# Kernel tuning notes

Hardware: AMD Instinct MI355X
Metric: run time of the kernel (lower is better)

The kernel has to match this reference:

```python
import jax, jax.numpy as jnp
import numpy as np

B, T, C = 4, 2048, 2048
H, KV, HD = 16, 4, 128  # n_head, n_kv_head, head_dim
G = H // KV             # query heads per kv head


def _rope(t, cos, sin):
    # t: [B, T, h, HD]; cos/sin: [T, HD//2] -> broadcast as [1, T, 1, HD//2]
    tr = t.reshape(t.shape[:-1] + (HD // 2, 2))
    t_r, t_i = tr[..., 0], tr[..., 1]
    c = cos[None, :, None, :]
    s = sin[None, :, None, :]
    o_r = t_r * c - t_i * s
    o_i = t_r * s + t_i * c
    return jnp.stack((o_r, o_i), axis=-1).reshape(t.shape)


def setup_inputs() -> dict:
    key = jax.random.key(0)
    ks = jax.random.split(key, 7)
    sc = 0.02
    return {
        "x": jax.random.normal(ks[0], (B, T, C), jnp.float32),
        "cos_freqs": jnp.cos(jnp.outer(jnp.arange(T, dtype=jnp.float32),
                                       1.0 / (10000.0 ** (jnp.arange(HD // 2, dtype=jnp.float32) * 2 / HD)))),
        "sin_freqs": jnp.sin(jnp.outer(jnp.arange(T, dtype=jnp.float32),
                                       1.0 / (10000.0 ** (jnp.arange(HD // 2, dtype=jnp.float32) * 2 / HD)))),
        "wq": jax.random.normal(ks[1], (H * HD, C), jnp.float32) * sc,
        "wk": jax.random.normal(ks[2], (KV * HD, C), jnp.float32) * sc,
        "wv": jax.random.normal(ks[3], (KV * HD, C), jnp.float32) * sc,
        "wo": jax.random.normal(ks[4], (C, H * HD), jnp.float32) * sc,
    }


def reference(x, cos_freqs, sin_freqs, wq, wk, wv, wo):
    # projections (Linear with bias=False: y = x @ W.T)
    q = (x @ wq.T).reshape(B, T, H, HD)
    k = (x @ wk.T).reshape(B, T, KV, HD)
    v = (x @ wv.T).reshape(B, T, KV, HD)
    q, k = _rope(q, cos_freqs, sin_freqs), _rope(k, cos_freqs, sin_freqs)
    # GQA attention without materializing repeated K/V: group q heads per kv head
    qg = q.reshape(B, T, KV, G, HD).transpose(0, 2, 3, 1, 4)  # [B,KV,G,T,HD]
    kh = k.transpose(0, 2, 1, 3)                              # [B,KV,T,HD]
    vh = v.transpose(0, 2, 1, 3)                              # [B,KV,T,HD]
    scale = 1.0 / jnp.sqrt(jnp.float32(HD))
    scores = jnp.einsum('bkgtd,bksd->bkgts', qg, kh) * scale  # [B,KV,G,T,T]
    mask = jnp.tril(jnp.ones((T, T), dtype=bool))
    scores = jnp.where(mask, scores, jnp.float32(-jnp.inf))
    attn = jax.nn.softmax(scores, axis=-1)
    out = jnp.einsum('bkgts,bksd->bkgtd', attn, vh)           # [B,KV,G,T,HD]
    out = out.transpose(0, 3, 1, 2, 4).reshape(B, T, H * HD)
    return out @ wo.T
```

## Files before the change

kernel.cpp:

```cpp
#include <hip/hip_runtime.h>
#include <hip/hip_bf16.h>
#include <math.h>

typedef __attribute__((ext_vector_type(8))) short short8;
typedef __attribute__((ext_vector_type(4))) float floatx4;

__device__ __forceinline__ float bf2f(unsigned short u) {
  union { unsigned int i; float f; } x; x.i = ((unsigned int)u) << 16; return x.f;
}
__device__ __forceinline__ unsigned short f2bf(float f) {
  union { float f; unsigned int i; } x; x.f = f;
  unsigned int r = x.i + 0x7FFFu + ((x.i >> 16) & 1u);
  return (unsigned short)(r >> 16);
}
__device__ __forceinline__ unsigned int pack2bf(float a, float b) {
  return (unsigned int)f2bf(a) | ((unsigned int)f2bf(b) << 16);
}
__device__ __forceinline__ void gl16(const void* g, void* l) {
  __builtin_amdgcn_global_load_lds(
      (const __attribute__((address_space(1))) unsigned int*)g,
      (__attribute__((address_space(3))) unsigned int*)l, 16, 0, 0);
}

__global__ void cvt_f32_bf16(const float* __restrict__ in, unsigned short* __restrict__ out, int n4) {
  int i = blockIdx.x * blockDim.x + threadIdx.x;
  if (i >= n4) return;
  float4 v = ((const float4*)in)[i];
  ushort4 o;
  o.x = f2bf(v.x); o.y = f2bf(v.y); o.z = f2bf(v.z); o.w = f2bf(v.w);
  ((ushort4*)out)[i] = o;
}

template<int MODE>
__global__ __launch_bounds__(256) void gemm_bt(const unsigned short* __restrict__ A,
                                               const unsigned short* __restrict__ Bw,
                                               void* __restrict__ out0,
                                               unsigned short* __restrict__ vtg,
                                               int M, int N, int K, int nbx) {
  __shared__ unsigned short SM[8192];
  unsigned short* As = SM;
  unsigned short* Bs = SM + 4096;
  const int nb = gridDim.x;
  const int bid = blockIdx.x;
  const int tile = (bid & 7) * (nb >> 3) + (bid >> 3);
  const int n0 = (tile % nbx) * 128, m0 = (tile / nbx) * 128;
  const int tid = threadIdx.x;
  const int lane = tid & 63, wave = tid >> 6;
  const int wm = wave >> 1, wn = wave & 1;
  const int r = lane & 15, g = lane >> 4;
  const int c8s = (lane & 3) * 8;
  const int rowbase = wave * 16 + (lane >> 2);
  floatx4 acc[4][4] = {};
  for (int k0 = 0; k0 < K; k0 += 32) {
    __syncthreads();
#pragma unroll
    for (int it = 0; it < 2; ++it) {
      int row = it * 64 + rowbase;
      gl16(A  + (size_t)(m0 + row) * K + k0 + c8s, (char*)As + it * 4096 + wave * 1024);
      gl16(Bw + (size_t)(n0 + row) * K + k0 + c8s, (char*)Bs + it * 4096 + wave * 1024);
    }
    asm volatile("s_waitcnt vmcnt(0)" ::: "memory");
    __syncthreads();
    short8 af[4], bf[4];
#pragma unroll
    for (int i = 0; i < 4; ++i) af[i] = *(const short8*)&As[(wm * 64 + i * 16 + r) * 32 + g * 8];
#pragma unroll
    for (int j = 0; j < 4; ++j) bf[j] = *(const short8*)&Bs[(wn * 64 + j * 16 + r) * 32 + g * 8];
#pragma unroll
    for (int i = 0; i < 4; ++i)
#pragma unroll
      for (int j = 0; j < 4; ++j)
        acc[i][j] = __builtin_amdgcn_mfma_f32_16x16x32_bf16(af[i], bf[j], acc[i][j], 0, 0, 0);
  }

  if (MODE == 0) {
    float* SMf = (float*)SM;
    float* outp = (float*)out0;
#pragma unroll
    for (int p = 0; p < 4; ++p) {
      __syncthreads();
      if (wm == (p >> 1)) {
#pragma unroll
        for (int i2 = 0; i2 < 2; ++i2) {
          int i = (p & 1) * 2 + i2;
#pragma unroll
          for (int j = 0; j < 4; ++j)
#pragma unroll
            for (int q = 0; q < 4; ++q)
              SMf[(i2 * 16 + g * 4 + q) * 128 + wn * 64 + j * 16 + r] = acc[i][j][q];
        }
      }
      __syncthreads();
#pragma unroll
      for (int it = 0; it < 4; ++it) {
        int c = it * 256 + tid;
        int row = c >> 5, c4 = c & 31;
        float4 v = *(float4*)&SMf[row * 128 + c4 * 4];
        *(float4*)(outp + (size_t)(m0 + p * 32 + row) * N + n0 + c4 * 4) = v;
      }
    }
  } else if (n0 < 2560) {
    unsigned short* outp = (unsigned short*)out0;
#pragma unroll
    for (int p = 0; p < 4; ++p) {
      __syncthreads();
      if (wm == (p >> 1)) {
#pragma unroll
        for (int i2 = 0; i2 < 2; ++i2) {
          int i = (p & 1) * 2 + i2;
#pragma unroll
          for (int j = 0; j < 4; ++j)
#pragma unroll
            for (int q = 0; q < 4; ++q)
              SM[(i2 * 16 + g * 4 + q) * 128 + wn * 64 + j * 16 + r] = f2bf(acc[i][j][q]);
        }
      }
      __syncthreads();
#pragma unroll
      for (int it = 0; it < 2; ++it) {
        int c = it * 256 + tid;
        int row = c >> 4, c8 = c & 15;
        short8 v = *(short8*)&SM[row * 128 + c8 * 8];
        *(short8*)(outp + (size_t)(m0 + p * 32 + row) * N + n0 + c8 * 8) = v;
      }
    }
  } else {
#pragma unroll
    for (int p = 0; p < 2; ++p) {
      __syncthreads();
      if (wn == p) {
#pragma unroll
        for (int i = 0; i < 4; ++i)
#pragma unroll
          for (int j = 0; j < 4; ++j)
#pragma unroll
            for (int q = 0; q < 4; ++q) {
              int ml = wm * 64 + i * 16 + g * 4 + q;
              int nl = j * 16 + r;
              SM[nl * 128 + (((ml >> 3) ^ (nl & 7)) << 3) + (ml & 7)] = f2bf(acc[i][j][q]);
            }
      }
      __syncthreads();
#pragma unroll
      for (int it = 0; it < 4; ++it) {
        int c = it * 256 + tid;
        int nl = c >> 4, m8 = c & 15;
        short8 v = *(short8*)&SM[nl * 128 + ((m8 ^ (nl & 7)) << 3)];
        *(short8*)(vtg + (size_t)(n0 - 2560 + p * 64 + nl) * 8192 + m0 + m8 * 8) = v;
      }
    }
  }
}

__global__ void rope_inplace(unsigned short* __restrict__ t,
                             const float* __restrict__ cosf, const float* __restrict__ sinf,
                             int heads, int rowStride, int total, float scale) {
  int i = blockIdx.x * blockDim.x + threadIdx.x;
  if (i >= total) return;
  int d8 = i & 15;
  int rem = i >> 4;
  int head = rem % heads;
  int tok = rem / heads;
  int tpos = tok & 2047;
  unsigned short* p = t + (size_t)tok * rowStride + head * 128 + d8 * 8;
  short8 v = *(short8*)p;
  float4 c = *(const float4*)(cosf + (size_t)tpos * 64 + d8 * 4);
  float4 s = *(const float4*)(sinf + (size_t)tpos * 64 + d8 * 4);
  float cc[4] = {c.x, c.y, c.z, c.w};
  float ss[4] = {s.x, s.y, s.z, s.w};
  short8 o;
#pragma unroll
  for (int j = 0; j < 4; ++j) {
    float tr = bf2f((unsigned short)v[2 * j]);
    float ti = bf2f((unsigned short)v[2 * j + 1]);
    float orr = (tr * cc[j] - ti * ss[j]) * scale;
    float oi  = (tr * ss[j] + ti * cc[j]) * scale;
    o[2 * j]     = (short)f2bf(orr);
    o[2 * j + 1] = (short)f2bf(oi);
  }
  *(short8*)p = o;
}

__global__ __launch_bounds__(256, 2) void attn_fwd(const unsigned short* __restrict__ QKV,
                                                   const unsigned short* __restrict__ VT,
                                                   unsigned short* __restrict__ O) {
  constexpr int T = 2048;
  constexpr int LDQ = 3072;
  constexpr float NEG = -1e30f;
  __shared__ unsigned short Ks[2][64 * 128];
  __shared__ unsigned short Vs[2][128 * 64];
  const int gid = blockIdx.x;
  const int hb  = gid & 63;
  const int p   = gid >> 6;
  const int h = hb & 15, b = hb >> 4;
  const int kvh = h >> 2;
  const int tid = threadIdx.x, lane = tid & 63, w = tid >> 6;
  const int r = lane & 15, g = lane >> 4;
  const int rbase = (r & 3) + ((r >> 2) << 3);
  const int swzr  = (r & 3) | (((r >> 2) & 1) << 2);
  const size_t bT = (size_t)b * T;

  const unsigned short* Kgb = QKV + bT * LDQ + 2048 + kvh * 128;
  const unsigned short* Vgb = VT + (size_t)(kvh * 128) * 8192 + b * 2048;

  auto STAGE = [&](int bi, int kv0) {
#pragma unroll
    for (int t2 = 0; t2 < 4; ++t2) {
      int ck = w * 4 + t2;
      { int row = ck * 4 + (lane >> 4); int c16 = lane & 15;
        int swz = (row & 3) | (((row >> 3) & 1) << 2);
        gl16(Kgb + (size_t)(kv0 + row) * LDQ + ((c16 ^ swz) << 3),
             (char*)(&Ks[bi][0]) + ck * 1024); }
      { int row = ck * 8 + (lane >> 3); int c16 = lane & 7;
        gl16(Vgb + (size_t)row * 8192 + kv0 + ((c16 ^ (row & 7)) << 3),
             (char*)(&Vs[bi][0]) + ck * 1024); }
    }
  };

  for (int seg = 0; seg < 2; ++seg) {
    const int qb = seg ? p : 15 - p;
    const int q0 = qb * 128;

    short8 qf[2][4];
#pragma unroll
    for (int qt = 0; qt < 2; ++qt) {
      const unsigned short* qp = QKV + (bT + q0 + w * 32 + qt * 16 + r) * LDQ + h * 128;
#pragma unroll
      for (int c = 0; c < 4; ++c) qf[qt][c] = *(const short8*)(qp + c * 32 + g * 8);
    }

    floatx4 acc[8][2] = {};
    float mrun[2] = {NEG, NEG};
    float lrun[2] = {0.f, 0.f};

    const int ntiles = (q0 + 128) >> 6;
    STAGE(0, 0);
    asm volatile("s_waitcnt vmcnt(0)" ::: "memory");
    __syncthreads();

    for (int t = 0; t < ntiles; ++t) {
      const int cur = t & 1;
      const int kv0 = t << 6;
      if (t + 1 < ntiles) STAGE(cur ^ 1, (t + 1) << 6);

      if (kv0 <= q0 + w * 32 + 31) {
        floatx4 st[2][4] = {};
        __builtin_amdgcn_s_setprio(1);
#pragma unroll
        for (int c = 0; c < 4; ++c) {
          short8 kf[4];
#pragma unroll
          for (int kt = 0; kt < 4; ++kt) {
            const int row = rbase + ((kt & 1) << 2) + ((kt >> 1) << 5);
            kf[kt] = *(const short8*)&Ks[cur][row * 128 + (((g + 4 * c) ^ swzr) << 3)];
          }
#pragma unroll
          for (int qt = 0; qt < 2; ++qt)
#pragma unroll
            for (int kt = 0; kt < 4; ++kt)
              st[qt][kt] = __builtin_amdgcn_mfma_f32_16x16x32_bf16(kf[kt], qf[qt][c], st[qt][kt], 0, 0, 0);
        }
        __builtin_amdgcn_s_setprio(0);

        short8 va[2][8];
#pragma unroll
        for (int kc = 0; kc < 2; ++kc)
#pragma unroll
          for (int dt = 0; dt < 8; ++dt)
            va[kc][dt] = *(const short8*)&Vs[cur][(dt * 16 + r) * 64 + (((g + 4 * kc) ^ (r & 7)) << 3)];

#pragma unroll
        for (int qt = 0; qt < 2; ++qt) {
          const int qmin = q0 + w * 32 + qt * 16;
          const int qrow = qmin + r;
          float x[4][4];
          bool needmask = (kv0 + 64 > qmin);
#pragma unroll
          for (int kt = 0; kt < 4; ++kt) {
            const int kvb = kv0 + ((kt >> 1) << 5) + (g << 3) + ((kt & 1) << 2);
#pragma unroll
            for (int j = 0; j < 4; ++j) {
              float v = st[qt][kt][j];
              if (needmask) v = (kvb + j <= qrow) ? v : NEG;
              x[kt][j] = v;
            }
          }
          float mloc = x[0][0];
#pragma unroll
          for (int kt = 0; kt < 4; ++kt)
#pragma unroll
            for (int j = 0; j < 4; ++j) mloc = fmaxf(mloc, x[kt][j]);
          mloc = fmaxf(mloc, __shfl_xor(mloc, 16));
          mloc = fmaxf(mloc, __shfl_xor(mloc, 32));
          if (!__all(mloc <= mrun[qt] + 8.f)) {
            float mnew = fmaxf(mrun[qt], mloc);
            float al = __expf(mrun[qt] - mnew);
            mrun[qt] = mnew;
            lrun[qt] *= al;
#pragma unroll
            for (int dt = 0; dt < 8; ++dt) acc[dt][qt] *= al;
          }
          float pr[4][4], ssum = 0.f;
#pragma unroll
          for (int kt = 0; kt < 4; ++kt)
#pragma unroll
            for (int j = 0; j < 4; ++j) { pr[kt][j] = __expf(x[kt][j] - mrun[qt]); ssum += pr[kt][j]; }
          ssum += __shfl_xor(ssum, 16);
          ssum += __shfl_xor(ssum, 32);
          lrun[qt] += ssum;
          uint2 pk[4];
#pragma unroll
          for (int kt = 0; kt < 4; ++kt) {
            pk[kt].x = pack2bf(pr[kt][0], pr[kt][1]);
            pk[kt].y = pack2bf(pr[kt][2], pr[kt][3]);
          }
          __builtin_amdgcn_s_setprio(1);
#pragma unroll
          for (int kc = 0; kc < 2; ++kc) {
            union { unsigned int u[4]; short8 s; } bw;
            bw.u[0] = pk[2 * kc].x;
            bw.u[1] = pk[2 * kc].y;
            bw.u[2] = pk[2 * kc + 1].x;
            bw.u[3] = pk[2 * kc + 1].y;
#pragma unroll
            for (int dt = 0; dt < 8; ++dt)
              acc[dt][qt] = __builtin_amdgcn_mfma_f32_16x16x32_bf16(va[kc][dt], bw.s, acc[dt][qt], 0, 0, 0);
          }
          __builtin_amdgcn_s_setprio(0);
        }
      }

      asm volatile("s_waitcnt vmcnt(0)" ::: "memory");
      __syncthreads();
    }

#pragma unroll
    for (int qt = 0; qt < 2; ++qt) {
      float inv = 1.f / lrun[qt];
      unsigned short* op = O + (bT + q0 + w * 32 + qt * 16 + r) * 2048 + h * 128;
#pragma unroll
      for (int dt = 0; dt < 8; ++dt) {
        uint2 pkd;
        pkd.x = pack2bf(acc[dt][qt][0] * inv, acc[dt][qt][1] * inv);
        pkd.y = pack2bf(acc[dt][qt][2] * inv, acc[dt][qt][3] * inv);
        *(uint2*)(op + dt * 16 + g * 4) = pkd;
      }
    }
  }
}

extern "C" void kernel_launch(void* const* d_in, const int* in_sizes, int n_in,
                              void* d_out, int out_size, void* d_ws, size_t ws_size,
                              hipStream_t stream) {
  const float* x    = (const float*)d_in[0];
  const float* cosf = (const float*)d_in[1];
  const float* sinf = (const float*)d_in[2];
  const float* wq   = (const float*)d_in[3];
  const float* wk   = (const float*)d_in[4];
  const float* wv   = (const float*)d_in[5];
  const float* wo   = (const float*)d_in[6];

  unsigned short* xb   = (unsigned short*)d_ws;
  unsigned short* qkvw = xb   + 16777216;
  unsigned short* wob  = qkvw + 6291456;
  unsigned short* qkv  = wob  + 4194304;
  unsigned short* Vtg  = qkv  + 25165824;
  unsigned short* AO   = Vtg  + 4194304;

  cvt_f32_bf16<<<16384, 256, 0, stream>>>(x,  xb,  4194304);
  cvt_f32_bf16<<<4096,  256, 0, stream>>>(wq, qkvw,           1048576);
  cvt_f32_bf16<<<1024,  256, 0, stream>>>(wk, qkvw + 4194304, 262144);
  cvt_f32_bf16<<<1024,  256, 0, stream>>>(wv, qkvw + 5242880, 262144);
  cvt_f32_bf16<<<4096,  256, 0, stream>>>(wo, wob, 1048576);

  gemm_bt<1><<<1536, 256, 0, stream>>>(xb, qkvw, qkv, Vtg, 8192, 3072, 2048, 24);

  rope_inplace<<<8192, 256, 0, stream>>>(qkv,        cosf, sinf, 16, 3072, 2097152, 0.08838834764831845f);
  rope_inplace<<<2048, 256, 0, stream>>>(qkv + 2048, cosf, sinf, 4,  3072, 524288,  1.0f);

  attn_fwd<<<512, 256, 0, stream>>>(qkv, Vtg, AO);

  gemm_bt<0><<<1024, 256, 0, stream>>>(AO, wob, d_out, nullptr, 8192, 2048, 2048, 16);
}
```

Measured before the change: 408.5 us.

## Triple-buffer GEMM LDS tiles with async prefetch and swizzled layout

Replaces the single-buffered GEMM main loop with a three-slot LDS ring. Global-to-LDS loads for tile t+2 are issued while tile t is being computed, so the vmcnt(0) wait before every iteration goes away. The LDS layout gets an XOR swizzle to reduce bank conflicts on the MFMA fragment reads, and s_setprio raises wave priority around the MFMA block. LDS use triples to 48KB and launch bounds now request 3 blocks per CU, which may limit occupancy or register allocation.

```diff
diff --git a/kernel.cpp b/kernel.cpp
--- a/kernel.cpp
+++ b/kernel.cpp
@@ -32,14 +32,12 @@
 }
 
 template<int MODE>
-__global__ __launch_bounds__(256) void gemm_bt(const unsigned short* __restrict__ A,
-                                               const unsigned short* __restrict__ Bw,
-                                               void* __restrict__ out0,
-                                               unsigned short* __restrict__ vtg,
-                                               int M, int N, int K, int nbx) {
-  __shared__ unsigned short SM[8192];
-  unsigned short* As = SM;
-  unsigned short* Bs = SM + 4096;
+__global__ __launch_bounds__(256, 3) void gemm_bt(const unsigned short* __restrict__ A,
+                                                  const unsigned short* __restrict__ Bw,
+                                                  void* __restrict__ out0,
+                                                  unsigned short* __restrict__ vtg,
+                                                  int M, int N, int K, int nbx) {
+  __shared__ __align__(16) unsigned short SM[24576];
   const int nb = gridDim.x;
   const int bid = blockIdx.x;
   const int tile = (bid & 7) * (nb >> 3) + (bid >> 3);
@@ -48,29 +46,64 @@
   const int lane = tid & 63, wave = tid >> 6;
   const int wm = wave >> 1, wn = wave & 1;
   const int r = lane & 15, g = lane >> 4;
-  const int c8s = (lane & 3) * 8;
-  const int rowbase = wave * 16 + (lane >> 2);
+  const int swzr = (r >> 1) & 3;
+
+  const int scg = (tid & 3) ^ ((tid >> 3) & 3);
+  const unsigned short* Arow = A + (size_t)(m0 + (tid >> 2)) * K + scg * 8;
+  const unsigned short* Brow = Bw + (size_t)(n0 + (tid >> 2)) * K + scg * 8;
+  const size_t K64 = (size_t)K * 64;
+  char* Lw = (char*)SM + wave * 1024;
+
+  const int aoff = (wm * 64 + r) * 32 + ((g ^ swzr) << 3);
+  const int boff = 4096 + (wn * 64 + r) * 32 + ((g ^ swzr) << 3);
+
+  auto STAGE = [&](int slot, int t) {
+    const unsigned short* Ag = Arow + ((size_t)t << 5);
+    const unsigned short* Bg = Brow + ((size_t)t << 5);
+    char* L = Lw + slot * 16384;
+    gl16(Ag,       L);
+    gl16(Ag + K64, L + 4096);
+    gl16(Bg,       L + 8192);
+    gl16(Bg + K64, L + 12288);
+  };
+
   floatx4 acc[4][4] = {};
-  for (int k0 = 0; k0 < K; k0 += 32) {
-    __syncthreads();
-#pragma unroll
-    for (int it = 0; it < 2; ++it) {
-      int row = it * 64 + rowbase;
-      gl16(A  + (size_t)(m0 + row) * K + k0 + c8s, (char*)As + it * 4096 + wave * 1024);
-      gl16(Bw + (size_t)(n0 + row) * K + k0 + c8s, (char*)Bs + it * 4096 + wave * 1024);
-    }
-    asm volatile("s_waitcnt vmcnt(0)" ::: "memory");
-    __syncthreads();
+  const int NT = K >> 5;
+
+  STAGE(0, 0);
+  STAGE(1, 1);
+  asm volatile("s_waitcnt vmcnt(4)" ::: "memory");
+  __builtin_amdgcn_s_barrier();
+  asm volatile("" ::: "memory");
+
+  int rd = 0, st = 2;
+  for (int t = 0; t < NT; ++t) {
+    const unsigned short* Ls = SM + rd * 8192;
     short8 af[4], bf[4];
 #pragma unroll
-    for (int i = 0; i < 4; ++i) af[i] = *(const short8*)&As[(wm * 64 + i * 16 + r) * 32 + g * 8];
-#pragma unroll
-    for (int j = 0; j < 4; ++j) bf[j] = *(const short8*)&Bs[(wn * 64 + j * 16 + r) * 32 + g * 8];
+    for (int i = 0; i < 4; ++i) af[i] = *(const short8*)&Ls[aoff + i * 512];
+#pragma unroll
+    for (int j = 0; j < 4; ++j) bf[j] = *(const short8*)&Ls[boff + j * 512];
+    if (t + 2 < NT) {
+      STAGE(st, t + 2);
+      asm volatile("s_waitcnt vmcnt(4)" ::: "memory");
+    } else if (t + 1 < NT) {
+      asm volatile("s_waitcnt vmcnt(0)" ::: "memory");
+    }
+    __builtin_amdgcn_s_barrier();
+    asm volatile("" ::: "memory");
+    __builtin_amdgcn_s_setprio(1);
 #pragma unroll
     for (int i = 0; i < 4; ++i)
 #pragma unroll
       for (int j = 0; j < 4; ++j)
         acc[i][j] = __builtin_amdgcn_mfma_f32_16x16x32_bf16(af[i], bf[j], acc[i][j], 0, 0, 0);
+    __builtin_amdgcn_s_setprio(0);
+    asm volatile("" ::: "memory");
+    __builtin_amdgcn_s_barrier();
+    asm volatile("" ::: "memory");
+    rd = rd == 2 ? 0 : rd + 1;
+    st = st == 2 ? 0 : st + 1;
   }
 
   if (MODE == 0) {
```

Result: faster. 387.8 us (-5.1%).
